# Kernel optimization log

Hardware: AMD Instinct MI355X
Metric: run time of the kernel (lower is better)

Reference implementation:

```python
import jax, jax.numpy as jnp
import numpy as np

DIM = 256
HEADS = 8
BALL = 128          # ball_size m
DIMENSIONALITY = 3
HIDDEN = 4 * DIM    # mlp_ratio * dim
HEAD_DIM = DIM // HEADS
EPS = 1e-6


def setup_inputs() -> dict:
    key = jax.random.key(0)
    ks = jax.random.split(key, 16)
    N = 131072
    s = lambda *sh: 1.0 / np.sqrt(sh[-1])
    inp = {
        "x": jax.random.normal(ks[0], (N, DIM), jnp.float32),
        "pos": jax.random.normal(ks[1], (N, DIMENSIONALITY), jnp.float32),
        "num_batches": 8,
        # BallMSA params
        "qkv_w": jax.random.normal(ks[2], (3 * DIM, DIM), jnp.float32) * s(DIM),
        "qkv_b": jnp.zeros((3 * DIM,), jnp.float32),
        "proj_w": jax.random.normal(ks[3], (DIM, DIM), jnp.float32) * s(DIM),
        "proj_b": jnp.zeros((DIM,), jnp.float32),
        "pe_w": jax.random.normal(ks[4], (DIM, DIMENSIONALITY), jnp.float32) * s(DIMENSIONALITY),
        "pe_b": jnp.zeros((DIM,), jnp.float32),
        "sigma_att": -1.0 + 0.01 * jax.random.normal(ks[5], (1, HEADS, 1, 1), jnp.float32),
        # norms
        "norm1_w": jnp.ones((DIM,), jnp.float32),
        "norm2_w": jnp.ones((DIM,), jnp.float32),
        # SwiGLU MLP
        "w1_w": jax.random.normal(ks[6], (HIDDEN, DIM), jnp.float32) * s(DIM),
        "w1_b": jnp.zeros((HIDDEN,), jnp.float32),
        "w2_w": jax.random.normal(ks[7], (HIDDEN, DIM), jnp.float32) * s(DIM),
        "w2_b": jnp.zeros((HIDDEN,), jnp.float32),
        "w3_w": jax.random.normal(ks[8], (DIM, HIDDEN), jnp.float32) * s(HIDDEN),
        "w3_b": jnp.zeros((DIM,), jnp.float32),
    }
    return inp


def _rmsnorm(x, w):
    return x * jax.lax.rsqrt(jnp.mean(x * x, axis=-1, keepdims=True) + EPS) * w


def _ball_msa(x, pos, qkv_w, qkv_b, proj_w, proj_b, pe_w, pe_b, sigma_att):
    N = x.shape[0]
    n = N // BALL
    p = pos.reshape(n, BALL, DIMENSIONALITY)
    # relative position wrt ball center (eq. 9), torch.no_grad in original
    rel = jax.lax.stop_gradient((p - p.mean(axis=1, keepdims=True)).reshape(N, DIMENSIONALITY))
    x = x + rel @ pe_w.T + pe_b
    # qkv: last dim laid out as (H E K) with K innermost
    qkv = (x @ qkv_w.T + qkv_b).reshape(n, BALL, HEADS, HEAD_DIM, 3)
    q = jnp.transpose(qkv[..., 0], (0, 2, 1, 3))  # n H m E
    k = jnp.transpose(qkv[..., 1], (0, 2, 1, 3))
    v = jnp.transpose(qkv[..., 2], (0, 2, 1, 3))
    # distance-based bias (eq. 10), torch.no_grad in original
    d = jnp.sqrt(jnp.sum((p[:, :, None, :] - p[:, None, :, :]) ** 2, axis=-1))  # n m m
    bias = jax.lax.stop_gradient(sigma_att[0]) * jax.lax.stop_gradient(d)[:, None, :, :]  # n H m m
    scores = jnp.einsum('nhme,nhke->nhmk', q, k) / np.sqrt(HEAD_DIM) + bias
    attn = jax.nn.softmax(scores, axis=-1)
    out = jnp.einsum('nhmk,nhke->nhme', attn, v)
    out = jnp.transpose(out, (0, 2, 1, 3)).reshape(N, DIM)  # (n m) (H E)
    return out @ proj_w.T + proj_b


def reference(x, pos, num_batches, qkv_w, qkv_b, proj_w, proj_b, pe_w, pe_b,
              sigma_att, norm1_w, norm2_w, w1_w, w1_b, w2_w, w2_b, w3_w, w3_b):
    # pre-norm block: x + BMSA(norm1(x)); x + SwiGLU(norm2(x))
    x = x + _ball_msa(_rmsnorm(x, norm1_w), pos, qkv_w, qkv_b, proj_w, proj_b,
                      pe_w, pe_b, sigma_att)
    h = _rmsnorm(x, norm2_w)
    gate = jax.nn.silu(h @ w1_w.T + w1_b)
    val = h @ w2_w.T + w2_b
    return x + (gate * val) @ w3_w.T + w3_b
```

## Files before the change

kernel.cpp:

```cpp
#include <hip/hip_runtime.h>

typedef __bf16 bf16x8 __attribute__((ext_vector_type(8)));
typedef float f32x4 __attribute__((ext_vector_type(4)));

__device__ __forceinline__ float b2f(unsigned short u) {
    union { unsigned int i; float f; } v; v.i = ((unsigned int)u) << 16; return v.f;
}
__device__ __forceinline__ unsigned short f2b(float f) {
    union { float f; unsigned int i; } v; v.f = f;
    unsigned int r = (v.i + 0x7fffu + ((v.i >> 16) & 1u)) >> 16;
    return (unsigned short)r;
}

__device__ __forceinline__ void gload16(const void* g, void* l) {
    __builtin_amdgcn_global_load_lds(
        (const __attribute__((address_space(1))) unsigned int*)g,
        (__attribute__((address_space(3))) unsigned int*)l,
        16, 0, 0);
}

__device__ __forceinline__ void xcd_map(int bid, int nx, int ny, int& bx, int& by) {
    if ((nx & 7) == 0) {
        int xcd = bid & 7;
        int s   = bid >> 3;
        int xl  = s / ny;
        by = s - xl * ny;
        bx = xcd * (nx >> 3) + xl;
    } else {
        bx = bid / ny;
        by = bid - bx * ny;
    }
}

__global__ __launch_bounds__(256)
void k_cvt5(const float* __restrict__ s0, const float* __restrict__ s1,
            const float* __restrict__ s2, const float* __restrict__ s3,
            const float* __restrict__ s4, unsigned short* __restrict__ dst)
{
    size_t gid = ((size_t)blockIdx.x * 256 + threadIdx.x) * 4;
    const float* src; size_t off;
    if      (gid < 196608) { src = s0; off = 0; }
    else if (gid < 262144) { src = s1; off = 196608; }
    else if (gid < 524288) { src = s2; off = 262144; }
    else if (gid < 786432) { src = s3; off = 524288; }
    else                   { src = s4; off = 786432; }
    float4 v = *(const float4*)(src + (gid - off));
    uint2 pk;
    pk.x = (unsigned int)f2b(v.x) | ((unsigned int)f2b(v.y) << 16);
    pk.y = (unsigned int)f2b(v.z) | ((unsigned int)f2b(v.w) << 16);
    *(uint2*)(dst + gid) = pk;
}

__global__ __launch_bounds__(256)
void k_norm1_pe(const float* __restrict__ x,
                const float* __restrict__ pos,
                const float* __restrict__ n1w,
                const float* __restrict__ pew,
                const float* __restrict__ peb,
                unsigned short* __restrict__ out)
{
    __shared__ float spw0[256], spw1[256], spw2[256], speb[256], snw[256];
    __shared__ float px[128], py[128], pz[128];
    __shared__ float mean[3];
    const int tid = threadIdx.x;
    const int ball = blockIdx.x;

    spw0[tid] = pew[tid*3+0]; spw1[tid] = pew[tid*3+1]; spw2[tid] = pew[tid*3+2];
    speb[tid] = peb[tid];     snw[tid]  = n1w[tid];
    if (tid < 128) {
        const float* pp = pos + (size_t)(ball*128 + tid)*3;
        px[tid] = pp[0]; py[tid] = pp[1]; pz[tid] = pp[2];
    }
    __syncthreads();
    if (tid < 3) {
        const float* arr = (tid==0) ? px : (tid==1) ? py : pz;
        float s = 0.f;
        for (int i = 0; i < 128; ++i) s += arr[i];
        mean[tid] = s * (1.0f/128.0f);
    }
    __syncthreads();

    const int wave = tid >> 6, lane = tid & 63;
    const float m0 = mean[0], m1 = mean[1], m2 = mean[2];
    for (int tok = wave; tok < 128; tok += 4) {
        size_t row = (size_t)(ball*128 + tok);
        float4 xv = *(const float4*)(x + row*256 + lane*4);
        float xf[4] = { xv.x, xv.y, xv.z, xv.w };
        float ss = xf[0]*xf[0] + xf[1]*xf[1] + xf[2]*xf[2] + xf[3]*xf[3];
        #pragma unroll
        for (int off = 1; off < 64; off <<= 1) ss += __shfl_xor(ss, off);
        float rstd = rsqrtf(ss * (1.0f/256.0f) + 1e-6f);
        float r0 = px[tok] - m0, r1 = py[tok] - m1, r2 = pz[tok] - m2;
        unsigned short o[4];
        #pragma unroll
        for (int k = 0; k < 4; ++k) {
            int j = lane*4 + k;
            float hv = xf[k] * rstd * snw[j];
            o[k] = f2b(hv + r0*spw0[j] + r1*spw1[j] + r2*spw2[j] + speb[j]);
        }
        uint2 pk;
        pk.x = (unsigned int)o[0] | ((unsigned int)o[1] << 16);
        pk.y = (unsigned int)o[2] | ((unsigned int)o[3] << 16);
        *(uint2*)(out + row*256 + lane*4) = pk;
    }
}

__global__ __launch_bounds__(256)
void k_rmsnorm(const float* __restrict__ x,
               const float* __restrict__ w,
               unsigned short* __restrict__ out)
{
    const int lane = threadIdx.x & 63;
    const size_t token = (size_t)blockIdx.x*4 + (threadIdx.x >> 6);
    float4 xv = *(const float4*)(x + token*256 + lane*4);
    float xf[4] = { xv.x, xv.y, xv.z, xv.w };
    float ss = xf[0]*xf[0] + xf[1]*xf[1] + xf[2]*xf[2] + xf[3]*xf[3];
    #pragma unroll
    for (int off = 1; off < 64; off <<= 1) ss += __shfl_xor(ss, off);
    float rstd = rsqrtf(ss * (1.0f/256.0f) + 1e-6f);
    float4 wv = *(const float4*)(w + lane*4);
    unsigned short o[4] = { f2b(xf[0]*rstd*wv.x), f2b(xf[1]*rstd*wv.y),
                            f2b(xf[2]*rstd*wv.z), f2b(xf[3]*rstd*wv.w) };
    uint2 pk;
    pk.x = (unsigned int)o[0] | ((unsigned int)o[1] << 16);
    pk.y = (unsigned int)o[2] | ((unsigned int)o[3] << 16);
    *(uint2*)(out + token*256 + lane*4) = pk;
}

__device__ __forceinline__ void gemm_mainloop_bt(
    const unsigned short* __restrict__ A, const unsigned short* __restrict__ B,
    int K, int m0, int n0, int tid,
    unsigned short* sA, unsigned short* sB, f32x4 (&acc)[4][4])
{
    const int lane = tid & 63;
    const int wave = tid >> 6;
    const int srow = wave * 32 + (lane >> 2);
    const int scol = (((lane & 3) ^ ((lane >> 3) & 3)) << 3);
    const unsigned short* pA = A + (size_t)(m0 + srow) * K + scol;
    const unsigned short* pB = B + (size_t)(n0 + srow) * K + scol;
    const size_t row16 = (size_t)16 * K;
    unsigned short* lA = sA + wave * 1024;
    unsigned short* lB = sB + wave * 1024;
    const int slot = ((lane & 15) << 2) | ((lane >> 4) ^ ((lane >> 1) & 3));
    const int aBase = (wave >> 1) * 2048 + slot * 8;
    const int bBase = (wave & 1) * 2048 + slot * 8;

    for (int k0 = 0; k0 < K; k0 += 32) {
        __syncthreads();
        gload16(pA + k0,         lA);
        gload16(pA + row16 + k0, lA + 512);
        gload16(pB + k0,         lB);
        gload16(pB + row16 + k0, lB + 512);
        __syncthreads();
        bf16x8 af[4], bfr[4];
        #pragma unroll
        for (int i = 0; i < 4; ++i) af[i]  = *(const bf16x8*)&sA[aBase + i*512];
        #pragma unroll
        for (int j = 0; j < 4; ++j) bfr[j] = *(const bf16x8*)&sB[bBase + j*512];
        #pragma unroll
        for (int i = 0; i < 4; ++i)
            #pragma unroll
            for (int j = 0; j < 4; ++j)
                acc[i][j] = __builtin_amdgcn_mfma_f32_16x16x32_bf16(af[i], bfr[j], acc[i][j], 0, 0, 0);
    }
}

__global__ __launch_bounds__(256, 2)
void k_gemm_bias(const unsigned short* __restrict__ A,
                 const unsigned short* __restrict__ B,
                 const float* __restrict__ bias,
                 const float* residual,
                 void* C, int K, int Ncols, int outBf16, int ny)
{
    __shared__ __align__(16) unsigned short sA[128*32];
    __shared__ __align__(16) unsigned short sB[128*32];
    const int tid = threadIdx.x;
    int bx, by;
    xcd_map(blockIdx.x, gridDim.x / ny, ny, bx, by);
    const int m0 = bx * 128, n0 = by * 128;
    f32x4 zero = {0.f, 0.f, 0.f, 0.f};
    f32x4 acc[4][4];
    #pragma unroll
    for (int i = 0; i < 4; ++i)
        #pragma unroll
        for (int j = 0; j < 4; ++j) acc[i][j] = zero;

    gemm_mainloop_bt(A, B, K, m0, n0, tid, sA, sB, acc);

    const int lane = tid & 63, lane16 = lane & 15, quad = lane >> 4;
    const int wave = tid >> 6, wm = (wave >> 1) * 64, wn = (wave & 1) * 64;
    #pragma unroll
    for (int i = 0; i < 4; ++i)
        #pragma unroll
        for (int j = 0; j < 4; ++j) {
            int n = n0 + wn + j*16 + lane16;
            float bj = bias[n];
            #pragma unroll
            for (int r = 0; r < 4; ++r) {
                int m = m0 + wm + i*16 + quad*4 + r;
                size_t idx = (size_t)m * Ncols + n;
                float v = acc[i][j][r] + bj;
                if (residual) v += residual[idx];
                if (outBf16) ((unsigned short*)C)[idx] = f2b(v);
                else         ((float*)C)[idx] = v;
            }
        }
}

__global__ __launch_bounds__(256, 3)
void k_gemm_swiglu(const unsigned short* __restrict__ A,
                   const unsigned short* __restrict__ B1,
                   const unsigned short* __restrict__ B2,
                   const float* __restrict__ b1,
                   const float* __restrict__ b2,
                   unsigned short* __restrict__ C, int K, int ny)
{
    __shared__ __align__(16) unsigned short sA[128*32];
    __shared__ __align__(16) unsigned short sB1[64*32];
    __shared__ __align__(16) unsigned short sB2[64*32];
    const int tid = threadIdx.x;
    int bx, by;
    xcd_map(blockIdx.x, gridDim.x / ny, ny, bx, by);
    const int m0 = bx * 128, n0 = by * 64;
    const int lane = tid & 63, lane16 = lane & 15, quad = lane >> 4;
    const int wave = tid >> 6;
    const int wm = (wave >> 1) * 64, wn = (wave & 1) * 32;
    const int srowA = wave * 32 + (lane >> 2);
    const int srowB = wave * 16 + (lane >> 2);
    const int scol  = (((lane & 3) ^ ((lane >> 3) & 3)) << 3);
    const unsigned short* pA  = A  + (size_t)(m0 + srowA) * K + scol;
    const unsigned short* pB1 = B1 + (size_t)(n0 + srowB) * K + scol;
    const unsigned short* pB2 = B2 + (size_t)(n0 + srowB) * K + scol;
    const size_t row16 = (size_t)16 * K;
    unsigned short* lA  = sA  + wave * 1024;
    unsigned short* lB1 = sB1 + wave * 512;
    unsigned short* lB2 = sB2 + wave * 512;
    const int slot = ((lane & 15) << 2) | ((lane >> 4) ^ ((lane >> 1) & 3));
    const int aBase = (wave >> 1) * 2048 + slot * 8;
    const int bBase = (wave & 1) * 1024 + slot * 8;

    f32x4 zero = {0.f, 0.f, 0.f, 0.f};
    f32x4 accg[4][2], accv[4][2];
    #pragma unroll
    for (int i = 0; i < 4; ++i)
        #pragma unroll
        for (int j = 0; j < 2; ++j) { accg[i][j] = zero; accv[i][j] = zero; }

    for (int k0 = 0; k0 < K; k0 += 32) {
        __syncthreads();
        gload16(pA + k0,         lA);
        gload16(pA + row16 + k0, lA + 512);
        gload16(pB1 + k0,        lB1);
        gload16(pB2 + k0,        lB2);
        __syncthreads();
        bf16x8 af[4], bg[2], bv[2];
        #pragma unroll
        for (int i = 0; i < 4; ++i) af[i] = *(const bf16x8*)&sA[aBase + i*512];
        #pragma unroll
        for (int j = 0; j < 2; ++j) {
            bg[j] = *(const bf16x8*)&sB1[bBase + j*512];
            bv[j] = *(const bf16x8*)&sB2[bBase + j*512];
        }
        #pragma unroll
        for (int i = 0; i < 4; ++i)
            #pragma unroll
            for (int j = 0; j < 2; ++j) {
                accg[i][j] = __builtin_amdgcn_mfma_f32_16x16x32_bf16(af[i], bg[j], accg[i][j], 0, 0, 0);
                accv[i][j] = __builtin_amdgcn_mfma_f32_16x16x32_bf16(af[i], bv[j], accv[i][j], 0, 0, 0);
            }
    }

    #pragma unroll
    for (int i = 0; i < 4; ++i)
        #pragma unroll
        for (int j = 0; j < 2; ++j) {
            int n = n0 + wn + j*16 + lane16;
            float bjg = b1[n], bjv = b2[n];
            #pragma unroll
            for (int r = 0; r < 4; ++r) {
                int m = m0 + wm + i*16 + quad*4 + r;
                float g  = accg[i][j][r] + bjg;
                float vv = accv[i][j][r] + bjv;
                float sg = 1.0f / (1.0f + __expf(-g));
                C[(size_t)m * 1024 + n] = f2b(g * sg * vv);
            }
        }
}

__global__ __launch_bounds__(256, 2)
void k_attn(const unsigned short* __restrict__ qkv,
            const float* __restrict__ pos,
            const float* __restrict__ sigma,
            unsigned short* __restrict__ out)
{
    __shared__ __align__(16) unsigned short Qs[128*40];
    __shared__ __align__(16) unsigned short Ks[128*40];
    __shared__ __align__(16) unsigned short Vt[32*136];
    __shared__ __align__(16) unsigned short Ps[128*136];
    __shared__ float px[128], py[128], pz[128];

    int ball, h;
    xcd_map(blockIdx.x, gridDim.x >> 3, 8, ball, h);
    const int tid  = threadIdx.x;

    {
        int tok = tid >> 1;
        int e0  = (tid & 1) * 16;
        const unsigned short* rowp = qkv + (size_t)(ball*128 + tok)*768 + h*96 + e0*3;
        unsigned short u[48];
        #pragma unroll
        for (int c = 0; c < 6; ++c) *(uint4*)&u[c*8] = *(const uint4*)(rowp + c*8);
        #pragma unroll
        for (int e = 0; e < 16; ++e) {
            Qs[tok*40 + e0 + e]    = u[e*3 + 0];
            Ks[tok*40 + e0 + e]    = u[e*3 + 1];
            Vt[(e0 + e)*136 + tok] = u[e*3 + 2];
        }
    }
    if (tid < 128) {
        const float* pp = pos + (size_t)(ball*128 + tid)*3;
        px[tid] = pp[0]; py[tid] = pp[1]; pz[tid] = pp[2];
    }
    __syncthreads();

    const int wave = tid >> 6, lane = tid & 63, lane16 = lane & 15, quad = lane >> 4;
    const float sig = sigma[h];
    const float scale = 0.17677669529663687f;
    f32x4 zero = {0.f, 0.f, 0.f, 0.f};

    f32x4 s[2][8];
    {
        bf16x8 a[2];
        #pragma unroll
        for (int i = 0; i < 2; ++i)
            a[i] = *(const bf16x8*)&Qs[(wave*32 + i*16 + lane16)*40 + quad*8];
        #pragma unroll
        for (int j = 0; j < 8; ++j) {
            bf16x8 b = *(const bf16x8*)&Ks[(j*16 + lane16)*40 + quad*8];
            #pragma unroll
            for (int i = 0; i < 2; ++i)
                s[i][j] = __builtin_amdgcn_mfma_f32_16x16x32_bf16(a[i], b, zero, 0, 0, 0);
        }
    }

    float pnx[8], pny[8], pnz[8];
    #pragma unroll
    for (int j = 0; j < 8; ++j) {
        int n = j*16 + lane16;
        pnx[j] = px[n]; pny[j] = py[n]; pnz[j] = pz[n];
    }
    float l[2][4];
    #pragma unroll
    for (int i = 0; i < 2; ++i)
        #pragma unroll
        for (int r = 0; r < 4; ++r) {
            int m = wave*32 + i*16 + quad*4 + r;
            float pmx = px[m], pmy = py[m], pmz = pz[m];
            float sv[8];
            float mx = -1e30f;
            #pragma unroll
            for (int j = 0; j < 8; ++j) {
                float dx = pmx - pnx[j], dy = pmy - pny[j], dz = pmz - pnz[j];
                float d = sqrtf(dx*dx + dy*dy + dz*dz);
                float val = s[i][j][r] * scale + sig * d;
                sv[j] = val;
                mx = fmaxf(mx, val);
            }
            #pragma unroll
            for (int off = 1; off < 16; off <<= 1) mx = fmaxf(mx, __shfl_xor(mx, off, 16));
            float sum = 0.f;
            #pragma unroll
            for (int j = 0; j < 8; ++j) {
                float p = __expf(sv[j] - mx);
                sum += p;
                Ps[(size_t)m*136 + j*16 + lane16] = f2b(p);
            }
            #pragma unroll
            for (int off = 1; off < 16; off <<= 1) sum += __shfl_xor(sum, off, 16);
            l[i][r] = sum;
        }
    __syncthreads();

    f32x4 o[2][2];
    #pragma unroll
    for (int i = 0; i < 2; ++i)
        #pragma unroll
        for (int nf = 0; nf < 2; ++nf) o[i][nf] = zero;
    #pragma unroll
    for (int c = 0; c < 4; ++c) {
        bf16x8 pa[2];
        #pragma unroll
        for (int i = 0; i < 2; ++i)
            pa[i] = *(const bf16x8*)&Ps[(wave*32 + i*16 + lane16)*136 + c*32 + quad*8];
        #pragma unroll
        for (int nf = 0; nf < 2; ++nf) {
            bf16x8 vb = *(const bf16x8*)&Vt[(nf*16 + lane16)*136 + c*32 + quad*8];
            #pragma unroll
            for (int i = 0; i < 2; ++i)
                o[i][nf] = __builtin_amdgcn_mfma_f32_16x16x32_bf16(pa[i], vb, o[i][nf], 0, 0, 0);
        }
    }

    #pragma unroll
    for (int i = 0; i < 2; ++i)
        #pragma unroll
        for (int nf = 0; nf < 2; ++nf)
            #pragma unroll
            for (int r = 0; r < 4; ++r) {
                int m = wave*32 + i*16 + quad*4 + r;
                out[(size_t)(ball*128 + m)*256 + h*32 + nf*16 + lane16] = f2b(o[i][nf][r] / l[i][r]);
            }
}

extern "C" void kernel_launch(void* const* d_in, const int* in_sizes, int n_in,
                              void* d_out, int out_size, void* d_ws, size_t ws_size,
                              hipStream_t stream)
{
    const float* x      = (const float*)d_in[0];
    const float* pos    = (const float*)d_in[1];
    const float* qkv_w  = (const float*)d_in[3];
    const float* qkv_b  = (const float*)d_in[4];
    const float* proj_w = (const float*)d_in[5];
    const float* proj_b = (const float*)d_in[6];
    const float* pe_w   = (const float*)d_in[7];
    const float* pe_b   = (const float*)d_in[8];
    const float* sigma  = (const float*)d_in[9];
    const float* n1w    = (const float*)d_in[10];
    const float* n2w    = (const float*)d_in[11];
    const float* w1w    = (const float*)d_in[12];
    const float* w1b    = (const float*)d_in[13];
    const float* w2w    = (const float*)d_in[14];
    const float* w2b    = (const float*)d_in[15];
    const float* w3w    = (const float*)d_in[16];
    const float* w3b    = (const float*)d_in[17];

    const int N = in_sizes[0] / 256;
    float* out = (float*)d_out;

    unsigned short* wb      = (unsigned short*)d_ws;
    unsigned short* qkv_wb  = wb;
    unsigned short* proj_wb = wb + 196608;
    unsigned short* w1wb    = wb + 262144;
    unsigned short* w2wb    = wb + 524288;
    unsigned short* w3wb    = wb + 786432;

    int C = 1;
    while (2097152 + (size_t)(N / C) * 2560 > ws_size && C < 256) C <<= 1;
    const int R = N / C;
    unsigned short* regA = wb + 1048576;
    unsigned short* regB = regA + (size_t)R * 1024;

    k_cvt5<<<1024, 256, 0, stream>>>(qkv_w, proj_w, w1w, w2w, w3w, wb);

    for (int c = 0; c < C; ++c) {
        const size_t row0 = (size_t)c * R;
        const float* x_c   = x   + row0 * 256;
        const float* pos_c = pos + row0 * 3;
        float* out_c = out + row0 * 256;
        const int nball_c = R / 128;
        const int nx = R / 128;

        k_norm1_pe<<<nball_c, 256, 0, stream>>>(x_c, pos_c, n1w, pe_w, pe_b, regB);
        k_gemm_bias<<<nx * 6, 256, 0, stream>>>(regB, qkv_wb, qkv_b, nullptr, regA, 256, 768, 1, 6);
        k_attn<<<nball_c * 8, 256, 0, stream>>>(regA, pos_c, sigma, regB);
        k_gemm_bias<<<nx * 2, 256, 0, stream>>>(regB, proj_wb, proj_b, x_c, out_c, 256, 256, 0, 2);
        k_rmsnorm<<<R/4, 256, 0, stream>>>(out_c, n2w, regB);
        k_gemm_swiglu<<<nx * 16, 256, 0, stream>>>(regB, w1wb, w2wb, w1b, w2b, regA, 256, 16);
        k_gemm_bias<<<nx * 2, 256, 0, stream>>>(regA, w3wb, w3b, out_c, out_c, 1024, 256, 0, 2);
    }
}
```

Before: 1.066 ms.

## Double-buffer LDS tiles in GEMM and SwiGLU GEMM main loops

Measured after the change: 1.078 ms. No clear change (+1.2%).

```diff
diff --git a/kernel.cpp b/kernel.cpp
--- a/kernel.cpp
+++ b/kernel.cpp
@@ -127,11 +127,37 @@
     *(uint2*)(out + token*256 + lane*4) = pk;
 }
 
-__device__ __forceinline__ void gemm_mainloop_bt(
-    const unsigned short* __restrict__ A, const unsigned short* __restrict__ B,
-    int K, int m0, int n0, int tid,
-    unsigned short* sA, unsigned short* sB, f32x4 (&acc)[4][4])
-{
+__device__ __forceinline__ void frag_mma16(
+    const unsigned short* cA, const unsigned short* cB,
+    int aBase, int bBase, f32x4 (&acc)[4][4])
+{
+    bf16x8 af[4], bfr[4];
+    #pragma unroll
+    for (int i = 0; i < 4; ++i) af[i]  = *(const bf16x8*)&cA[aBase + i*512];
+    #pragma unroll
+    for (int j = 0; j < 4; ++j) bfr[j] = *(const bf16x8*)&cB[bBase + j*512];
+    #pragma unroll
+    for (int i = 0; i < 4; ++i)
+        #pragma unroll
+        for (int j = 0; j < 4; ++j)
+            acc[i][j] = __builtin_amdgcn_mfma_f32_16x16x32_bf16(af[i], bfr[j], acc[i][j], 0, 0, 0);
+}
+
+__global__ __launch_bounds__(256, 2)
+void k_gemm_bias(const unsigned short* __restrict__ A,
+                 const unsigned short* __restrict__ B,
+                 const float* __restrict__ bias,
+                 const float* residual,
+                 void* C, int K, int Ncols, int outBf16, int ny)
+{
+    __shared__ __align__(16) unsigned short sA0[128*32];
+    __shared__ __align__(16) unsigned short sB0[128*32];
+    __shared__ __align__(16) unsigned short sA1[128*32];
+    __shared__ __align__(16) unsigned short sB1[128*32];
+    const int tid = threadIdx.x;
+    int bx, by;
+    xcd_map(blockIdx.x, gridDim.x / ny, ny, bx, by);
+    const int m0 = bx * 128, n0 = by * 128;
     const int lane = tid & 63;
     const int wave = tid >> 6;
     const int srow = wave * 32 + (lane >> 2);
@@ -139,45 +165,11 @@
     const unsigned short* pA = A + (size_t)(m0 + srow) * K + scol;
     const unsigned short* pB = B + (size_t)(n0 + srow) * K + scol;
     const size_t row16 = (size_t)16 * K;
-    unsigned short* lA = sA + wave * 1024;
-    unsigned short* lB = sB + wave * 1024;
+    const int stO = wave * 1024;
     const int slot = ((lane & 15) << 2) | ((lane >> 4) ^ ((lane >> 1) & 3));
     const int aBase = (wave >> 1) * 2048 + slot * 8;
     const int bBase = (wave & 1) * 2048 + slot * 8;
 
-    for (int k0 = 0; k0 < K; k0 += 32) {
-        __syncthreads();
-        gload16(pA + k0,         lA);
-        gload16(pA + row16 + k0, lA + 512);
-        gload16(pB + k0,         lB);
-        gload16(pB + row16 + k0, lB + 512);
-        __syncthreads();
-        bf16x8 af[4], bfr[4];
-        #pragma unroll
-        for (int i = 0; i < 4; ++i) af[i]  = *(const bf16x8*)&sA[aBase + i*512];
-        #pragma unroll
-        for (int j = 0; j < 4; ++j) bfr[j] = *(const bf16x8*)&sB[bBase + j*512];
-        #pragma unroll
-        for (int i = 0; i < 4; ++i)
-            #pragma unroll
-            for (int j = 0; j < 4; ++j)
-                acc[i][j] = __builtin_amdgcn_mfma_f32_16x16x32_bf16(af[i], bfr[j], acc[i][j], 0, 0, 0);
-    }
-}
-
-__global__ __launch_bounds__(256, 2)
-void k_gemm_bias(const unsigned short* __restrict__ A,
-                 const unsigned short* __restrict__ B,
-                 const float* __restrict__ bias,
-                 const float* residual,
-                 void* C, int K, int Ncols, int outBf16, int ny)
-{
-    __shared__ __align__(16) unsigned short sA[128*32];
-    __shared__ __align__(16) unsigned short sB[128*32];
-    const int tid = threadIdx.x;
-    int bx, by;
-    xcd_map(blockIdx.x, gridDim.x / ny, ny, bx, by);
-    const int m0 = bx * 128, n0 = by * 128;
     f32x4 zero = {0.f, 0.f, 0.f, 0.f};
     f32x4 acc[4][4];
     #pragma unroll
@@ -185,10 +177,32 @@
         #pragma unroll
         for (int j = 0; j < 4; ++j) acc[i][j] = zero;
 
-    gemm_mainloop_bt(A, B, K, m0, n0, tid, sA, sB, acc);
-
-    const int lane = tid & 63, lane16 = lane & 15, quad = lane >> 4;
-    const int wave = tid >> 6, wm = (wave >> 1) * 64, wn = (wave & 1) * 64;
+    gload16(pA, sA0 + stO);  gload16(pA + row16, sA0 + stO + 512);
+    gload16(pB, sB0 + stO);  gload16(pB + row16, sB0 + stO + 512);
+    __syncthreads();
+
+    const int nt = K >> 5;
+    for (int t = 0; t < nt; t += 2) {
+        const int k1 = (t + 1) << 5;
+        gload16(pA + k1,         sA1 + stO);
+        gload16(pA + row16 + k1, sA1 + stO + 512);
+        gload16(pB + k1,         sB1 + stO);
+        gload16(pB + row16 + k1, sB1 + stO + 512);
+        frag_mma16(sA0, sB0, aBase, bBase, acc);
+        __syncthreads();
+        if (t + 2 < nt) {
+            const int k2 = (t + 2) << 5;
+            gload16(pA + k2,         sA0 + stO);
+            gload16(pA + row16 + k2, sA0 + stO + 512);
+            gload16(pB + k2,         sB0 + stO);
+            gload16(pB + row16 + k2, sB0 + stO + 512);
+        }
+        frag_mma16(sA1, sB1, aBase, bBase, acc);
+        __syncthreads();
+    }
+
+    const int lane16 = lane & 15, quad = lane >> 4;
+    const int wm = (wave >> 1) * 64, wn = (wave & 1) * 64;
     #pragma unroll
     for (int i = 0; i < 4; ++i)
         #pragma unroll
@@ -207,6 +221,27 @@
         }
 }
 
+__device__ __forceinline__ void frag_mma_dual(
+    const unsigned short* cA, const unsigned short* cB1, const unsigned short* cB2,
+    int aBase, int bBase, f32x4 (&accg)[4][2], f32x4 (&accv)[4][2])
+{
+    bf16x8 af[4], bg[2], bv[2];
+    #pragma unroll
+    for (int i = 0; i < 4; ++i) af[i] = *(const bf16x8*)&cA[aBase + i*512];
+    #pragma unroll
+    for (int j = 0; j < 2; ++j) {
+        bg[j] = *(const bf16x8*)&cB1[bBase + j*512];
+        bv[j] = *(const bf16x8*)&cB2[bBase + j*512];
+    }
+    #pragma unroll
+    for (int i = 0; i < 4; ++i)
+        #pragma unroll
+        for (int j = 0; j < 2; ++j) {
+            accg[i][j] = __builtin_amdgcn_mfma_f32_16x16x32_bf16(af[i], bg[j], accg[i][j], 0, 0, 0);
+            accv[i][j] = __builtin_amdgcn_mfma_f32_16x16x32_bf16(af[i], bv[j], accv[i][j], 0, 0, 0);
+        }
+}
+
 __global__ __launch_bounds__(256, 3)
 void k_gemm_swiglu(const unsigned short* __restrict__ A,
                    const unsigned short* __restrict__ B1,
@@ -215,9 +250,12 @@
                    const float* __restrict__ b2,
                    unsigned short* __restrict__ C, int K, int ny)
 {
-    __shared__ __align__(16) unsigned short sA[128*32];
-    __shared__ __align__(16) unsigned short sB1[64*32];
-    __shared__ __align__(16) unsigned short sB2[64*32];
+    __shared__ __align__(16) unsigned short sA0[128*32];
+    __shared__ __align__(16) unsigned short sA1[128*32];
+    __shared__ __align__(16) unsigned short sB10[64*32];
+    __shared__ __align__(16) unsigned short sB11[64*32];
+    __shared__ __align__(16) unsigned short sB20[64*32];
+    __shared__ __align__(16) unsigned short sB21[64*32];
     const int tid = threadIdx.x;
     int bx, by;
     xcd_map(blockIdx.x, gridDim.x / ny, ny, bx, by);
@@ -232,9 +270,8 @@
     const unsigned short* pB1 = B1 + (size_t)(n0 + srowB) * K + scol;
     const unsigned short* pB2 = B2 + (size_t)(n0 + srowB) * K + scol;
     const size_t row16 = (size_t)16 * K;
-    unsigned short* lA  = sA  + wave * 1024;
-    unsigned short* lB1 = sB1 + wave * 512;
-    unsigned short* lB2 = sB2 + wave * 512;
+    const int stA = wave * 1024;
+    const int stB = wave * 512;
     const int slot = ((lane & 15) << 2) | ((lane >> 4) ^ ((lane >> 1) & 3));
     const int aBase = (wave >> 1) * 2048 + slot * 8;
     const int bBase = (wave & 1) * 1024 + slot * 8;
@@ -246,28 +283,29 @@
         #pragma unroll
         for (int j = 0; j < 2; ++j) { accg[i][j] = zero; accv[i][j] = zero; }
 
-    for (int k0 = 0; k0 < K; k0 += 32) {
+    gload16(pA, sA0 + stA);  gload16(pA + row16, sA0 + stA + 512);
+    gload16(pB1, sB10 + stB);
+    gload16(pB2, sB20 + stB);
+    __syncthreads();
+
+    const int nt = K >> 5;
+    for (int t = 0; t < nt; t += 2) {
+        const int k1 = (t + 1) << 5;
+        gload16(pA + k1,         sA1 + stA);
+        gload16(pA + row16 + k1, sA1 + stA + 512);
+        gload16(pB1 + k1,        sB11 + stB);
+        gload16(pB2 + k1,        sB21 + stB);
+        frag_mma_dual(sA0, sB10, sB20, aBase, bBase, accg, accv);
         __syncthreads();
-        gload16(pA + k0,         lA);
-        gload16(pA + row16 + k0, lA + 512);
-        gload16(pB1 + k0,        lB1);
-        gload16(pB2 + k0,        lB2);
+        if (t + 2 < nt) {
+            const int k2 = (t + 2) << 5;
+            gload16(pA + k2,         sA0 + stA);
+            gload16(pA + row16 + k2, sA0 + stA + 512);
+            gload16(pB1 + k2,        sB10 + stB);
+            gload16(pB2 + k2,        sB20 + stB);
+        }
+        frag_mma_dual(sA1, sB11, sB21, aBase, bBase, accg, accv);
         __syncthreads();
-        bf16x8 af[4], bg[2], bv[2];
-        #pragma unroll
-        for (int i = 0; i < 4; ++i) af[i] = *(const bf16x8*)&sA[aBase + i*512];
-        #pragma unroll
-        for (int j = 0; j < 2; ++j) {
-            bg[j] = *(const bf16x8*)&sB1[bBase + j*512];
-            bv[j] = *(const bf16x8*)&sB2[bBase + j*512];
-        }
-        #pragma unroll
-        for (int i = 0; i < 4; ++i)
-            #pragma unroll
-            for (int j = 0; j < 2; ++j) {
-                accg[i][j] = __builtin_amdgcn_mfma_f32_16x16x32_bf16(af[i], bg[j], accg[i][j], 0, 0, 0);
-                accv[i][j] = __builtin_amdgcn_mfma_f32_16x16x32_bf16(af[i], bv[j], accv[i][j], 0, 0, 0);
-            }
     }
 
     #pragma unroll
```
